# Kernel optimization log

Hardware: AMD Instinct MI355X
Metric: run time of the kernel (lower is better)

Reference implementation:

```python
import jax, jax.numpy as jnp
import numpy as np

VOXEL_DIM = 16
Z_BINS = 64
BEV_DIM = 64
LN_EPS = 1e-5


def setup_inputs() -> dict:
    key = jax.random.key(0)
    ks = jax.random.split(key, 6)
    B, H, W, Z, C = 1, 256, 256, Z_BINS, VOXEL_DIM
    dense_volume = jax.random.normal(ks[0], (B, H, W, Z, C), dtype=jnp.float32)
    # learned params
    z_embed = jax.random.normal(ks[1], (Z_BINS, VOXEL_DIM), dtype=jnp.float32)
    w1 = jax.random.normal(ks[2], (2 * VOXEL_DIM, BEV_DIM), dtype=jnp.float32) * (1.0 / np.sqrt(2 * VOXEL_DIM))
    b1 = jax.random.normal(ks[3], (BEV_DIM,), dtype=jnp.float32) * 0.01
    ln_gamma = jnp.ones((BEV_DIM,), dtype=jnp.float32)
    ln_beta = jnp.zeros((BEV_DIM,), dtype=jnp.float32)
    return {
        "dense_volume": dense_volume,
        "z_embed": z_embed,
        "w1": w1,
        "b1": b1,
        "ln_gamma": ln_gamma,
        "ln_beta": ln_beta,
    }


def reference(dense_volume, z_embed, w1, b1, ln_gamma, ln_beta):
    # dense_volume: (B,H,W,Z,C); z_embed: (Z,C) broadcast over B,H,W
    # concat [voxel, z_emb] -> linear(2C -> bev) + relu
    # Split the matmul to avoid materializing the concatenated (B,H,W,Z,2C) tensor:
    # cat([v, e]) @ w1 == v @ w1[:C] + e @ w1[C:]
    C = dense_volume.shape[-1]
    w_v, w_e = w1[:C], w1[C:]
    # z-embedding contribution: (Z, bev) — computed once, broadcast
    z_part = jnp.einsum("zc,cd->zd", z_embed, w_e) + b1
    x = jnp.einsum("bhwzc,cd->bhwzd", dense_volume, w_v) + z_part  # (B,H,W,Z,bev)
    x = jax.nn.relu(x)
    x = x.sum(axis=3)  # sum over Z pillars -> (B,H,W,bev)
    # LayerNorm over last dim
    mean = x.mean(axis=-1, keepdims=True)
    var = x.var(axis=-1, keepdims=True)
    x = (x - mean) * jax.lax.rsqrt(var + LN_EPS)
    return x * ln_gamma + ln_beta
```

## Files before the change

kernel.cpp:

```cpp
#include <hip/hip_runtime.h>
#include <hip/hip_bf16.h>

typedef short bf16x8 __attribute__((ext_vector_type(8)));
typedef float floatx4 __attribute__((ext_vector_type(4)));

union U128 { bf16x8 h; __hip_bfloat16 e[8]; };

__device__ __forceinline__ bf16x8 cvt8(const float4& a, const float4& b) {
  U128 u;
  u.e[0] = __float2bfloat16(a.x); u.e[1] = __float2bfloat16(a.y);
  u.e[2] = __float2bfloat16(a.z); u.e[3] = __float2bfloat16(a.w);
  u.e[4] = __float2bfloat16(b.x); u.e[5] = __float2bfloat16(b.y);
  u.e[6] = __float2bfloat16(b.z); u.e[7] = __float2bfloat16(b.w);
  return u.h;
}

__global__ __launch_bounds__(256, 2) void bev_kernel(
    const float* __restrict__ dv,
    const float* __restrict__ ze,
    const float* __restrict__ w1,
    const float* __restrict__ b1,
    const float* __restrict__ gam,
    const float* __restrict__ bet,
    float* __restrict__ out,
    int P)
{
  const int lane = threadIdx.x & 63;
  const int wid  = blockIdx.x * (blockDim.x >> 6) + (threadIdx.x >> 6);
  const int nw   = gridDim.x * (blockDim.x >> 6);
  const int q = lane >> 4;
  const int m = lane & 15;

  bf16x8 bfrag[4];
  #pragma unroll
  for (int nb = 0; nb < 4; ++nb) {
    U128 t;
    #pragma unroll
    for (int j = 0; j < 8; ++j)
      t.e[j] = __float2bfloat16(w1[(q * 8 + j) * 64 + nb * 16 + m]);
    bfrag[nb] = t.h;
  }
  floatx4 cinit[4];
  #pragma unroll
  for (int nb = 0; nb < 4; ++nb) {
    float b = b1[nb * 16 + m];
    cinit[nb] = (floatx4){b, b, b, b};
  }
  const float gl = gam[lane];
  const float bl = bet[lane];

  bf16x8 aez[4];
  #pragma unroll
  for (int t = 0; t < 4; ++t) {
    const char* zp = (const char*)ze + 1024 * t + 64 * m + 32 * (q & 1);
    aez[t] = cvt8(*(const float4*)zp, *(const float4*)(zp + 16));
  }

  const char* p = (const char*)dv + (long)wid * 4096 + 64 * m + 32 * (q & 1);
  const long step = (long)nw * 4096;

  float4 curA[8], nxtA[8];
  int pix = wid;
  if (pix < P && q < 2) {
    #pragma unroll
    for (int t = 0; t < 4; ++t) {
      curA[2 * t]     = *(const float4*)(p + 1024 * t);
      curA[2 * t + 1] = *(const float4*)(p + 1024 * t + 16);
    }
  }
  for (; pix < P; pix += nw) {
    p += step;
    if (q < 2 && pix + nw < P) {
      #pragma unroll
      for (int t = 0; t < 4; ++t) {
        nxtA[2 * t]     = *(const float4*)(p + 1024 * t);
        nxtA[2 * t + 1] = *(const float4*)(p + 1024 * t + 16);
      }
    }

    float acc[4] = {0.f, 0.f, 0.f, 0.f};
    #pragma unroll
    for (int t = 0; t < 4; ++t) {
      U128 a;
      if (q < 2) a.h = cvt8(curA[2 * t], curA[2 * t + 1]);
      else       a.h = aez[t];
      #pragma unroll
      for (int nb = 0; nb < 4; ++nb) {
        floatx4 d = __builtin_amdgcn_mfma_f32_16x16x32_bf16(a.h, bfrag[nb], cinit[nb], 0, 0, 0);
        acc[nb] += (fmaxf(d[0], 0.f) + fmaxf(d[1], 0.f)) +
                   (fmaxf(d[2], 0.f) + fmaxf(d[3], 0.f));
      }
    }
    #pragma unroll
    for (int nb = 0; nb < 4; ++nb) {
      acc[nb] += __shfl_xor(acc[nb], 16, 64);
      acc[nb] += __shfl_xor(acc[nb], 32, 64);
    }
    float s  = acc[0] + acc[1] + acc[2] + acc[3];
    float sq = acc[0]*acc[0] + acc[1]*acc[1] + acc[2]*acc[2] + acc[3]*acc[3];
    #pragma unroll
    for (int off = 1; off <= 8; off <<= 1) {
      s  += __shfl_xor(s, off, 64);
      sq += __shfl_xor(sq, off, 64);
    }
    const float mean = s * 0.015625f;
    const float var  = sq * 0.015625f - mean * mean;
    const float rs   = rsqrtf(var + 1e-5f);
    const float v = (q == 0) ? acc[0] : (q == 1) ? acc[1] : (q == 2) ? acc[2] : acc[3];
    out[(long)pix * 64 + lane] = (v - mean) * rs * gl + bl;

    #pragma unroll
    for (int t = 0; t < 8; ++t) curA[t] = nxtA[t];
  }
}

extern "C" void kernel_launch(void* const* d_in, const int* in_sizes, int n_in,
                              void* d_out, int out_size, void* d_ws, size_t ws_size,
                              hipStream_t stream) {
  const float* dv  = (const float*)d_in[0];
  const float* ze  = (const float*)d_in[1];
  const float* w1  = (const float*)d_in[2];
  const float* b1  = (const float*)d_in[3];
  const float* gam = (const float*)d_in[4];
  const float* bet = (const float*)d_in[5];
  float* out = (float*)d_out;

  const int P = in_sizes[0] / (64 * 16);
  dim3 grid(2048), block(256);
  bev_kernel<<<grid, block, 0, stream>>>(dv, ze, w1, b1, gam, bet, out, P);
}
```

Measured before the change: 366.7 us.

## Process two pixels per wave with all lanes loading and a bit-trick bf16 pack

Each wave now handles two pixels per iteration. Lanes 32-63, which previously sat idle during loads, now fetch the second pixel's voxels, and a second weight fragment with permuted rows lets them reuse the same MFMA layout with the z-embedding half swapped. The bf16 conversion becomes a manual round-to-nearest-even bit pack, and the prefetched data is converted to bf16 at the end of the loop instead of being copied as floats. Launch bounds move to 3 blocks per SM. This roughly halves loop iterations and evens out load bandwidth across lanes, at the cost of more registers and twice the MFMAs per iteration. It also assumes P is even.

```diff
diff --git a/kernel.cpp b/kernel.cpp
--- a/kernel.cpp
+++ b/kernel.cpp
@@ -4,18 +4,23 @@
 typedef short bf16x8 __attribute__((ext_vector_type(8)));
 typedef float floatx4 __attribute__((ext_vector_type(4)));
 
-union U128 { bf16x8 h; __hip_bfloat16 e[8]; };
+union F8 { bf16x8 h; unsigned u[4]; };
+
+__device__ __forceinline__ unsigned pk(float lo, float hi) {
+  unsigned a = __float_as_uint(lo), b = __float_as_uint(hi);
+  a += 0x7fffu + ((a >> 16) & 1u);
+  b += 0x7fffu + ((b >> 16) & 1u);
+  return (a >> 16) | (b & 0xffff0000u);
+}
 
 __device__ __forceinline__ bf16x8 cvt8(const float4& a, const float4& b) {
-  U128 u;
-  u.e[0] = __float2bfloat16(a.x); u.e[1] = __float2bfloat16(a.y);
-  u.e[2] = __float2bfloat16(a.z); u.e[3] = __float2bfloat16(a.w);
-  u.e[4] = __float2bfloat16(b.x); u.e[5] = __float2bfloat16(b.y);
-  u.e[6] = __float2bfloat16(b.z); u.e[7] = __float2bfloat16(b.w);
+  F8 u;
+  u.u[0] = pk(a.x, a.y); u.u[1] = pk(a.z, a.w);
+  u.u[2] = pk(b.x, b.y); u.u[3] = pk(b.z, b.w);
   return u.h;
 }
 
-__global__ __launch_bounds__(256, 2) void bev_kernel(
+__global__ __launch_bounds__(256, 3) void bev_kernel(
     const float* __restrict__ dv,
     const float* __restrict__ ze,
     const float* __restrict__ w1,
@@ -31,14 +36,19 @@
   const int q = lane >> 4;
   const int m = lane & 15;
 
-  bf16x8 bfrag[4];
+  bf16x8 bA[4], bB[4];
   #pragma unroll
   for (int nb = 0; nb < 4; ++nb) {
-    U128 t;
+    const int col = nb * 16 + m;
+    F8 ta, tb;
     #pragma unroll
-    for (int j = 0; j < 8; ++j)
-      t.e[j] = __float2bfloat16(w1[(q * 8 + j) * 64 + nb * 16 + m]);
-    bfrag[nb] = t.h;
+    for (int i = 0; i < 4; ++i) {
+      const int rA = q * 8 + 2 * i;
+      ta.u[i] = pk(w1[rA * 64 + col], w1[(rA + 1) * 64 + col]);
+      const int rB0 = (rA + 16) & 31, rB1 = (rA + 17) & 31;
+      tb.u[i] = pk(w1[rB0 * 64 + col], w1[rB1 * 64 + col]);
+    }
+    bA[nb] = ta.h; bB[nb] = tb.h;
   }
   floatx4 cinit[4];
   #pragma unroll
@@ -56,61 +66,77 @@
     aez[t] = cvt8(*(const float4*)zp, *(const float4*)(zp + 16));
   }
 
-  const char* p = (const char*)dv + (long)wid * 4096 + 64 * m + 32 * (q & 1);
-  const long step = (long)nw * 4096;
+  const char* p = (const char*)dv + (long)wid * 8192 +
+                  (q >= 2 ? 4096 : 0) + 64 * m + 32 * (q & 1);
+  const long step = (long)nw * 8192;
 
-  float4 curA[8], nxtA[8];
-  int pix = wid;
-  if (pix < P && q < 2) {
+  float4 r[8];
+  bf16x8 frag[4];
+  int u = wid;
+  if (2 * u < P) {
     #pragma unroll
     for (int t = 0; t < 4; ++t) {
-      curA[2 * t]     = *(const float4*)(p + 1024 * t);
-      curA[2 * t + 1] = *(const float4*)(p + 1024 * t + 16);
+      r[2 * t]     = *(const float4*)(p + 1024 * t);
+      r[2 * t + 1] = *(const float4*)(p + 1024 * t + 16);
     }
+    #pragma unroll
+    for (int t = 0; t < 4; ++t) frag[t] = cvt8(r[2 * t], r[2 * t + 1]);
   }
-  for (; pix < P; pix += nw) {
+
+  for (; 2 * u < P; u += nw) {
     p += step;
-    if (q < 2 && pix + nw < P) {
+    if (2 * (u + nw) < P) {
       #pragma unroll
       for (int t = 0; t < 4; ++t) {
-        nxtA[2 * t]     = *(const float4*)(p + 1024 * t);
-        nxtA[2 * t + 1] = *(const float4*)(p + 1024 * t + 16);
+        r[2 * t]     = *(const float4*)(p + 1024 * t);
+        r[2 * t + 1] = *(const float4*)(p + 1024 * t + 16);
       }
     }
 
-    float acc[4] = {0.f, 0.f, 0.f, 0.f};
+    float a0[4] = {0.f, 0.f, 0.f, 0.f};
+    float a1[4] = {0.f, 0.f, 0.f, 0.f};
     #pragma unroll
     for (int t = 0; t < 4; ++t) {
-      U128 a;
-      if (q < 2) a.h = cvt8(curA[2 * t], curA[2 * t + 1]);
-      else       a.h = aez[t];
+      const bf16x8 A0 = (q < 2) ? frag[t] : aez[t];
+      const bf16x8 A1 = (q < 2) ? aez[t] : frag[t];
       #pragma unroll
       for (int nb = 0; nb < 4; ++nb) {
-        floatx4 d = __builtin_amdgcn_mfma_f32_16x16x32_bf16(a.h, bfrag[nb], cinit[nb], 0, 0, 0);
-        acc[nb] += (fmaxf(d[0], 0.f) + fmaxf(d[1], 0.f)) +
-                   (fmaxf(d[2], 0.f) + fmaxf(d[3], 0.f));
+        floatx4 d0 = __builtin_amdgcn_mfma_f32_16x16x32_bf16(A0, bA[nb], cinit[nb], 0, 0, 0);
+        a0[nb] += (fmaxf(d0[0], 0.f) + fmaxf(d0[1], 0.f)) +
+                  (fmaxf(d0[2], 0.f) + fmaxf(d0[3], 0.f));
+        floatx4 d1 = __builtin_amdgcn_mfma_f32_16x16x32_bf16(A1, bB[nb], cinit[nb], 0, 0, 0);
+        a1[nb] += (fmaxf(d1[0], 0.f) + fmaxf(d1[1], 0.f)) +
+                  (fmaxf(d1[2], 0.f) + fmaxf(d1[3], 0.f));
       }
     }
     #pragma unroll
     for (int nb = 0; nb < 4; ++nb) {
-      acc[nb] += __shfl_xor(acc[nb], 16, 64);
-      acc[nb] += __shfl_xor(acc[nb], 32, 64);
+      a0[nb] += __shfl_xor(a0[nb], 16, 64);
+      a1[nb] += __shfl_xor(a1[nb], 16, 64);
+      a0[nb] += __shfl_xor(a0[nb], 32, 64);
+      a1[nb] += __shfl_xor(a1[nb], 32, 64);
     }
-    float s  = acc[0] + acc[1] + acc[2] + acc[3];
-    float sq = acc[0]*acc[0] + acc[1]*acc[1] + acc[2]*acc[2] + acc[3]*acc[3];
+    float s0 = a0[0] + a0[1] + a0[2] + a0[3];
+    float s1 = a1[0] + a1[1] + a1[2] + a1[3];
+    float q0 = a0[0]*a0[0] + a0[1]*a0[1] + a0[2]*a0[2] + a0[3]*a0[3];
+    float q1 = a1[0]*a1[0] + a1[1]*a1[1] + a1[2]*a1[2] + a1[3]*a1[3];
     #pragma unroll
     for (int off = 1; off <= 8; off <<= 1) {
-      s  += __shfl_xor(s, off, 64);
-      sq += __shfl_xor(sq, off, 64);
+      s0 += __shfl_xor(s0, off, 64);
+      s1 += __shfl_xor(s1, off, 64);
+      q0 += __shfl_xor(q0, off, 64);
+      q1 += __shfl_xor(q1, off, 64);
     }
-    const float mean = s * 0.015625f;
-    const float var  = sq * 0.015625f - mean * mean;
-    const float rs   = rsqrtf(var + 1e-5f);
-    const float v = (q == 0) ? acc[0] : (q == 1) ? acc[1] : (q == 2) ? acc[2] : acc[3];
-    out[(long)pix * 64 + lane] = (v - mean) * rs * gl + bl;
+    const float mean0 = s0 * 0.015625f, mean1 = s1 * 0.015625f;
+    const float rs0 = rsqrtf(q0 * 0.015625f - mean0 * mean0 + 1e-5f);
+    const float rs1 = rsqrtf(q1 * 0.015625f - mean1 * mean1 + 1e-5f);
+    const float v0 = (q == 0) ? a0[0] : (q == 1) ? a0[1] : (q == 2) ? a0[2] : a0[3];
+    const float v1 = (q == 0) ? a1[0] : (q == 1) ? a1[1] : (q == 2) ? a1[2] : a1[3];
+    out[(long)u * 128 + lane]      = (v0 - mean0) * rs0 * gl + bl;
+    out[(long)u * 128 + 64 + lane] = (v1 - mean1) * rs1 * gl + bl;
 
     #pragma unroll
-    for (int t = 0; t < 8; ++t) curA[t] = nxtA[t];
+    for (int t = 0; t < 4; ++t) frag[t] = cvt8(r[2 * t], r[2 * t + 1]);
   }
 }
 
```

Result: slower. 377.2 us (+2.9%).
